# Optimization experiments

Measured on AMD Instinct MI355X. Metric: run time of the kernel, lower is better.

The kernel has to match this reference:

```python
import jax, jax.numpy as jnp
import numpy as np

B, T, H = 512, 200, 512


def setup_inputs() -> dict:
    key = jax.random.key(0)
    ks = jax.random.split(key, 9)
    s = 0.05  # small init to avoid gate saturation
    return {
        "inp": jax.random.normal(ks[0], (B, T), dtype=jnp.float32),
        "Wx1": jax.random.normal(ks[1], (1, 4 * H), dtype=jnp.float32) * s,
        "Wh1": jax.random.normal(ks[2], (H, 4 * H), dtype=jnp.float32) * s,
        "b1": jax.random.normal(ks[3], (4 * H,), dtype=jnp.float32) * s,
        "Wx2": jax.random.normal(ks[4], (H, 4 * H), dtype=jnp.float32) * s,
        "Wh2": jax.random.normal(ks[5], (H, 4 * H), dtype=jnp.float32) * s,
        "b2": jax.random.normal(ks[6], (4 * H,), dtype=jnp.float32) * s,
        "Wfc": jax.random.normal(ks[7], (H, 1), dtype=jnp.float32) * s,
        "bfc": jax.random.normal(ks[8], (1,), dtype=jnp.float32) * s,
    }


def _lstm(x_seq, Wx, Wh, b, h0, c0):
    # x_seq: [B, T, Din]; precompute input projection for all steps
    xz = jnp.einsum("btd,dg->btg", x_seq, Wx) + b  # [B, T, 4H]
    h_dim = Wh.shape[0]

    def step(carry, xz_t):
        h, c = carry
        z = xz_t + h @ Wh  # [B, 4H]
        i, f, g, o = jnp.split(z, 4, axis=-1)  # keras gate order i,f,g,o
        i = jax.nn.sigmoid(i)
        f = jax.nn.sigmoid(f)
        g = jnp.tanh(g)
        o = jax.nn.sigmoid(o)
        c = f * c + i * g
        h = o * jnp.tanh(c)
        return (h, c), h

    (hf, cf), hs = jax.lax.scan(step, (h0, c0), jnp.swapaxes(xz, 0, 1))
    return jnp.swapaxes(hs, 0, 1), hf, cf  # seq [B,T,H], final h, final c


def reference(inp, Wx1, Wh1, b1, Wx2, Wh2, b2, Wfc, bfc):
    b, t = inp.shape
    h = Wh1.shape[0]
    x = inp[..., None]  # [B, T, 1]
    z0 = jnp.zeros((b, h), dtype=inp.dtype)
    seq1, h1, c1 = _lstm(x, Wx1, Wh1, b1, z0, z0)
    # lstm2 is seeded with lstm1's final (h, c) because the [seq,h,c] list
    # is passed directly to the second keras LSTM layer
    seq2, h2, c2 = _lstm(seq1, Wx2, Wh2, b2, h1, c1)
    logits = h2 @ Wfc + bfc  # [B, 1]
    return logits
```

## Files before the change

kernel.cpp:

```cpp
#include <hip/hip_runtime.h>
#include <cstdio>

typedef __attribute__((ext_vector_type(8))) short short8;
typedef __attribute__((ext_vector_type(4))) float f32x4;
typedef unsigned long long u64;

#define MFMA16(a,b,c) __builtin_amdgcn_mfma_f32_16x16x32_bf16((a),(b),(c),0,0,0)
#define LOAD_SYS(p)    __hip_atomic_load((p), __ATOMIC_RELAXED, __HIP_MEMORY_SCOPE_SYSTEM)
#define STORE_SYS(p,v) __hip_atomic_store((p), (v), __ATOMIC_RELAXED, __HIP_MEMORY_SCOPE_SYSTEM)

typedef __attribute__((address_space(1))) unsigned AS1U;
typedef __attribute__((address_space(3))) unsigned AS3U;

constexpr size_t CNT_OFF = 0;
constexpr size_t HB_OFF  = 8192;
constexpr size_t PK1_OFF = HB_OFF + 1048576;
constexpr size_t PK2_OFF = PK1_OFF + 2097152;
constexpr size_t PKX_OFF = PK2_OFF + 2097152;
constexpr size_t SEQ_OFF = PKX_OFF + 2097152;
constexpr size_t WS_NEED = SEQ_OFF + 16ul * 200 * 32768;

__device__ __forceinline__ short f2bf(float f) {
  union { float f; unsigned u; } v; v.f = f;
  unsigned r = v.u + 0x7fffu + ((v.u >> 16) & 1u);
  return (short)(r >> 16);
}
__device__ __forceinline__ float bf2f(short s) {
  union { float f; unsigned u; } v; v.u = ((unsigned)(unsigned short)s) << 16;
  return v.f;
}
__device__ __forceinline__ float sigm(float x)   { return 1.f / (1.f + __expf(-x)); }
__device__ __forceinline__ float tanh_f(float x) { return 1.f - 2.f / (1.f + __expf(2.f * x)); }

__global__ void pack_w(const float* __restrict__ wh1, const float* __restrict__ wh2,
                       const float* __restrict__ wx2, unsigned char* __restrict__ ws)
{
  int tid = blockIdx.x * 256 + threadIdx.x;
  int m   = tid >> 16;
  int rem = tid & 65535;
  int k   = rem >> 7;
  int nf  = rem & 127;
  const float* W = (m == 0) ? wh1 : (m == 1) ? wh2 : wx2;
  short* dst = (short*)(ws + ((m == 0) ? PK1_OFF : (m == 1) ? PK2_OFF : PKX_OFF));
  int kf = k >> 5, sub = (k >> 3) & 3, e = k & 7;
  int base = ((nf * 16 + kf) * 64 + sub * 16) * 8 + e;
  const float* src = W + (size_t)k * 2048 + nf * 16;
#pragma unroll
  for (int c = 0; c < 16; ++c) dst[base + c * 8] = f2bf(src[c]);
}

__global__ __launch_bounds__(256, 1) void lstm_main(
    const float* __restrict__ inp, const float* __restrict__ Wx1,
    const float* __restrict__ b1,  const float* __restrict__ b2,
    const float* __restrict__ Wfc, const float* __restrict__ bfc,
    unsigned char* __restrict__ ws, float* __restrict__ out)
{
  __shared__ short8 ldsA[2048];
  __shared__ short8 ldsB[2048];
  __shared__ short8 bwx[4][2][8][64];
  __shared__ float  zlds[32][132];
  __shared__ unsigned short htile[32][36];
  __shared__ float  red[256];

  const int tid  = threadIdx.x;
  const int blk  = blockIdx.x;
  const int gr   = blk & 15;
  const int wj   = blk >> 4;
  const int w    = tid >> 6;
  const int lane = tid & 63;
  const int g0   = (w >> 1) << 1;
  const int cf   = w & 1;

  unsigned* fl = (unsigned*)(ws + CNT_OFF) + gr * 32;
  short8* hb0p = (short8*)(ws + HB_OFF) + (size_t)(0 * 16 + gr) * 2048;
  short8* hb1p = (short8*)(ws + HB_OFF) + (size_t)(1 * 16 + gr) * 2048;
  const short8* pk1 = (const short8*)(ws + PK1_OFF);
  const short8* pk2 = (const short8*)(ws + PK2_OFF);
  const short8* pkx = (const short8*)(ws + PKX_OFF);
  short8* seq = (short8*)(ws + SEQ_OFF) + (size_t)gr * (200 * 2048);

  short8 wh1f[2][16], wh2f[2][16], wxhi[2][8];
#pragma unroll
  for (int Gl = 0; Gl < 2; ++Gl) {
    int nf = (g0 + Gl) * 32 + wj * 2 + cf;
#pragma unroll
    for (int kf = 0; kf < 16; ++kf) {
      wh1f[Gl][kf] = pk1[(nf * 16 + kf) * 64 + lane];
      wh2f[Gl][kf] = pk2[(nf * 16 + kf) * 64 + lane];
    }
#pragma unroll
    for (int kf = 0; kf < 8; ++kf)
      bwx[w][Gl][kf][lane] = pkx[(nf * 16 + kf) * 64 + lane];
#pragma unroll
    for (int kf = 8; kf < 16; ++kf)
      wxhi[Gl][kf - 8] = pkx[(nf * 16 + kf) * 64 + lane];
  }

  const int hcol = tid & 31, rq = tid >> 5;
  const int jcol = wj * 32 + hcol;
  float wx1v[4], b1v[4], b2v[4];
#pragma unroll
  for (int G = 0; G < 4; ++G) {
    wx1v[G] = Wx1[G * 512 + jcol];
    b1v[G]  = b1[G * 512 + jcol];
    b2v[G]  = b2[G * 512 + jcol];
  }
  const float* xptr = inp + (size_t)(gr * 32 + rq * 4) * 200;

  const int pr = tid >> 3, pq = tid & 7;
  const int pc0 = wj * 32 + pq * 4;
  const int bq = ((((pc0 >> 5) * 2 + (pr >> 4)) * 64 + ((pc0 >> 3) & 3) * 16 + (pr & 15)) * 8
                  + (pc0 & 7)) >> 2;

  float cst1[4] = {0.f, 0.f, 0.f, 0.f};
  float cst2[4] = {0.f, 0.f, 0.f, 0.f};

  __syncthreads();

#pragma unroll 1
  for (int s = 0; s <= 200; ++s) {
    float xv[4];
    if (s < 200) {
#pragma unroll
      for (int i = 0; i < 4; ++i) xv[i] = xptr[i * 200 + s];
    }

    if (s > 0) {
      if (tid < 64) {
        const unsigned* fp = &fl[tid & 15];
        while (1) {
          unsigned v = LOAD_SYS((unsigned*)fp);
          if (__all((int)(v >= (unsigned)s))) break;
          __builtin_amdgcn_s_sleep(1);
        }
        asm volatile("" ::: "memory");
      }
    }
    __syncthreads();

    if (s >= 1) {
      const char* gsrc = (const char*)(seq + (size_t)(s - 1) * 2048);
      char* ldst = (char*)ldsA;
#pragma unroll
      for (int i = 0; i < 8; ++i)
        __builtin_amdgcn_global_load_lds(
            (const AS1U*)(gsrc + (w * 8 + i) * 1024 + lane * 16),
            (AS3U*)(ldst + (w * 8 + i) * 1024), 16, 0, 17 );
    }
    if (s >= 2) {
      const char* gsrc = (const char*)((s & 1) ? hb1p : hb0p);
      char* ldst = (char*)ldsB;
#pragma unroll
      for (int i = 0; i < 8; ++i)
        __builtin_amdgcn_global_load_lds(
            (const AS1U*)(gsrc + (w * 8 + i) * 1024 + lane * 16),
            (AS3U*)(ldst + (w * 8 + i) * 1024), 16, 0, 17);
    }
    __builtin_amdgcn_sched_barrier(0);
    if (s >= 2) asm volatile("s_waitcnt vmcnt(8)" ::: "memory");
    else        asm volatile("s_waitcnt vmcnt(0)" ::: "memory");
    __builtin_amdgcn_sched_barrier(0);
    __builtin_amdgcn_s_barrier();

    f32x4 acc1[2][2], acc2[2][2];
#pragma unroll
    for (int Gl = 0; Gl < 2; ++Gl)
#pragma unroll
      for (int m = 0; m < 2; ++m) {
        f32x4 z = {0.f, 0.f, 0.f, 0.f}; acc1[Gl][m] = z; acc2[Gl][m] = z;
      }

    if (s >= 1) {
#pragma unroll
      for (int m = 0; m < 2; ++m) {
#pragma unroll
        for (int kf = 0; kf < 16; ++kf) {
          short8 a = ldsA[(kf * 2 + m) * 64 + lane];
#pragma unroll
          for (int Gl = 0; Gl < 2; ++Gl) {
            if (s < 200) acc1[Gl][m] = MFMA16(a, wh1f[Gl][kf], acc1[Gl][m]);
            short8 bx = (kf < 8) ? bwx[w][Gl][kf][lane] : wxhi[Gl][kf - 8];
            acc2[Gl][m] = MFMA16(a, bx, acc2[Gl][m]);
          }
        }
      }
    }

    if (s < 200) {
#pragma unroll
      for (int Gl = 0; Gl < 2; ++Gl)
#pragma unroll
        for (int m = 0; m < 2; ++m)
#pragma unroll
          for (int r = 0; r < 4; ++r)
            zlds[m * 16 + (lane >> 4) * 4 + r][(g0 + Gl) * 32 + cf * 16 + (lane & 15)]
                = acc1[Gl][m][r];
    }
    __syncthreads();

    if (s < 200) {
#pragma unroll
      for (int i = 0; i < 4; ++i) {
        int row = rq * 4 + i;
        float zi = zlds[row][0 * 32 + hcol] + fmaf(xv[i], wx1v[0], b1v[0]);
        float zf = zlds[row][1 * 32 + hcol] + fmaf(xv[i], wx1v[1], b1v[1]);
        float zg = zlds[row][2 * 32 + hcol] + fmaf(xv[i], wx1v[2], b1v[2]);
        float zo = zlds[row][3 * 32 + hcol] + fmaf(xv[i], wx1v[3], b1v[3]);
        float cc = sigm(zf) * cst1[i] + sigm(zi) * tanh_f(zg);
        cst1[i] = cc;
        htile[row][hcol] = (unsigned short)f2bf(sigm(zo) * tanh_f(cc));
      }
    }

    if (s >= 2) {
#pragma unroll
      for (int m = 0; m < 2; ++m) {
#pragma unroll
        for (int kf = 0; kf < 16; ++kf) {
          short8 a = ldsB[(kf * 2 + m) * 64 + lane];
#pragma unroll
          for (int Gl = 0; Gl < 2; ++Gl)
            acc2[Gl][m] = MFMA16(a, wh2f[Gl][kf], acc2[Gl][m]);
        }
      }
    }
    __syncthreads();

    if (s < 200) {
      u64 hv = *(const u64*)&htile[pr][pq * 4];
      STORE_SYS((u64*)(seq + (size_t)s * 2048) + bq, hv);
    }

    if (s >= 1) {
#pragma unroll
      for (int Gl = 0; Gl < 2; ++Gl)
#pragma unroll
        for (int m = 0; m < 2; ++m)
#pragma unroll
          for (int r = 0; r < 4; ++r)
            zlds[m * 16 + (lane >> 4) * 4 + r][(g0 + Gl) * 32 + cf * 16 + (lane & 15)]
                = acc2[Gl][m][r];
    }
    __syncthreads();

    if (s >= 1) {
#pragma unroll
      for (int i = 0; i < 4; ++i) {
        int row = rq * 4 + i;
        float zi = zlds[row][0 * 32 + hcol] + b2v[0];
        float zf = zlds[row][1 * 32 + hcol] + b2v[1];
        float zg = zlds[row][2 * 32 + hcol] + b2v[2];
        float zo = zlds[row][3 * 32 + hcol] + b2v[3];
        float cc = sigm(zf) * cst2[i] + sigm(zi) * tanh_f(zg);
        cst2[i] = cc;
        htile[row][hcol] = (unsigned short)f2bf(sigm(zo) * tanh_f(cc));
      }
    }
    __syncthreads();

    if (s >= 1) {
      u64 hv = *(const u64*)&htile[pr][pq * 4];
      short8* dst = (s & 1) ? hb0p : hb1p;
      STORE_SYS((u64*)dst + bq, hv);
    }
    __syncthreads();
    if (tid == 0)
      STORE_SYS(&fl[wj], (unsigned)(s + 1));
  }

  if (wj == 0) {
    if (tid < 64) {
      const unsigned* fp = &fl[tid & 15];
      while (1) {
        unsigned v = LOAD_SYS((unsigned*)fp);
        if (__all((int)(v >= 201u))) break;
        __builtin_amdgcn_s_sleep(1);
      }
      asm volatile("" ::: "memory");
    }
    __syncthreads();

    const u64* h2 = (const u64*)hb1p;
    int r = tid >> 3, q = tid & 7;
    float sum = 0.f;
#pragma unroll
    for (int c = 0; c < 8; ++c) {
      int k0 = q * 64 + c * 8;
      int kf = k0 >> 5, sub = (k0 >> 3) & 3, m = r >> 4;
      int bq2 = ((kf * 2 + m) * 64 + sub * 16 + (r & 15)) * 2;
      union { u64 u[2]; unsigned short ss[8]; } cv;
      cv.u[0] = LOAD_SYS((u64*)h2 + bq2);
      cv.u[1] = LOAD_SYS((u64*)h2 + bq2 + 1);
#pragma unroll
      for (int e = 0; e < 8; ++e)
        sum = fmaf(bf2f((short)cv.ss[e]), Wfc[k0 + e], sum);
    }
    red[tid] = sum;
    __syncthreads();
    if (q == 0) {
      float o = bfc[0];
#pragma unroll
      for (int j = 0; j < 8; ++j) o += red[r * 8 + j];
      out[gr * 32 + r] = o;
    }
  }
}

extern "C" void kernel_launch(void* const* d_in, const int* in_sizes, int n_in,
                              void* d_out, int out_size, void* d_ws, size_t ws_size,
                              hipStream_t stream)
{
  if (ws_size < WS_NEED) {
    fprintf(stderr, "kernel_launch: ws_size %zu < needed %zu\n", ws_size, WS_NEED);
    return;
  }
  const float* inp = (const float*)d_in[0];
  const float* Wx1 = (const float*)d_in[1];
  const float* Wh1 = (const float*)d_in[2];
  const float* b1  = (const float*)d_in[3];
  const float* Wx2 = (const float*)d_in[4];
  const float* Wh2 = (const float*)d_in[5];
  const float* b2  = (const float*)d_in[6];
  const float* Wfc = (const float*)d_in[7];
  const float* bfc = (const float*)d_in[8];
  unsigned char* ws = (unsigned char*)d_ws;

  hipMemsetAsync(ws, 0, 8192, stream);
  pack_w<<<768, 256, 0, stream>>>(Wh1, Wh2, Wx2, ws);
  lstm_main<<<256, 256, 0, stream>>>(inp, Wx1, b1, b2, Wfc, bfc, ws, (float*)d_out);
}
```

Baseline: 1.451 ms.

## Split each block's batch tile into two ping-pong halves to overlap sync with compute

Each workgroup now handles two 16-row batch subgroups (A and B) instead of one 32-row group. It alternates phases, so one subgroup's global-to-LDS staging and cross-block wait overlap the other subgroup's MFMA and gate work. Layer-1 and layer-2 gate computations are also fused into a single pass per phase, cutting the number of barriers. Per-block flag arrays are replaced by one atomic counter per subgroup. The cost is half-height MFMA tiles, so the weight registers are reused less per step, and the per-step atomic counters may contend.

Measured after the change: 2.581 ms. 77.8% more time.

```diff
diff --git a/kernel.cpp b/kernel.cpp
--- a/kernel.cpp
+++ b/kernel.cpp
@@ -18,7 +18,7 @@
 constexpr size_t PK2_OFF = PK1_OFF + 2097152;
 constexpr size_t PKX_OFF = PK2_OFF + 2097152;
 constexpr size_t SEQ_OFF = PKX_OFF + 2097152;
-constexpr size_t WS_NEED = SEQ_OFF + 16ul * 200 * 32768;
+constexpr size_t WS_NEED = SEQ_OFF + 32ul * 200 * 16384;
 
 __device__ __forceinline__ short f2bf(float f) {
   union { float f; unsigned u; } v; v.f = f;
@@ -49,35 +49,144 @@
   for (int c = 0; c < 16; ++c) dst[base + c * 8] = f2bf(src[c]);
 }
 
+__device__ __forceinline__ void stage16k(const char* g, char* l, int w, int lane) {
+#pragma unroll
+  for (int i = 0; i < 4; ++i)
+    __builtin_amdgcn_global_load_lds(
+        (const AS1U*)(g + (w * 4 + i) * 1024 + lane * 16),
+        (AS3U*)(l + (w * 4 + i) * 1024), 16, 0, 17 );
+}
+
+#define LGKM_BAR() do { \
+  asm volatile("s_waitcnt lgkmcnt(0)" ::: "memory"); \
+  __builtin_amdgcn_s_barrier(); \
+  __builtin_amdgcn_sched_barrier(0); } while (0)
+
+__device__ __forceinline__ void phase_step(
+    int s, int tid, int lane, int w, int g0, int cf,
+    const short8* tA, const short8* tB,
+    const short8 (&wh1f)[2][16], const short8 (&wh2f)[2][16],
+    const short8 (&wxhi)[2][8], const short8 (&bwx)[4][2][8][64],
+    float (&zl1)[16][132], float (&zl2)[16][132],
+    unsigned short (&ht1)[16][36], unsigned short (&ht2)[16][36],
+    const float* xg, const float (&wx1v)[4], const float (&b1v)[4], const float (&b2v)[4],
+    float (&c1)[2], float (&c2)[2],
+    u64* seqG, u64* hbG0, u64* hbG1,
+    int pr, int pq, int bq, unsigned* cnt)
+{
+  f32x4 a1[2], a2[2];
+#pragma unroll
+  for (int Gl = 0; Gl < 2; ++Gl) { f32x4 z = {0.f,0.f,0.f,0.f}; a1[Gl] = z; a2[Gl] = z; }
+
+  if (s >= 1) {
+#pragma unroll
+    for (int kf = 0; kf < 16; ++kf) {
+      short8 a = tA[kf * 64 + lane];
+#pragma unroll
+      for (int Gl = 0; Gl < 2; ++Gl) {
+        if (s < 200) a1[Gl] = MFMA16(a, wh1f[Gl][kf], a1[Gl]);
+        short8 bxf = (kf < 8) ? bwx[w][Gl][kf][lane] : wxhi[Gl][kf - 8];
+        a2[Gl] = MFMA16(a, bxf, a2[Gl]);
+      }
+    }
+  }
+  if (s >= 2) {
+#pragma unroll
+    for (int kf = 0; kf < 16; ++kf) {
+      short8 b = tB[kf * 64 + lane];
+#pragma unroll
+      for (int Gl = 0; Gl < 2; ++Gl)
+        a2[Gl] = MFMA16(b, wh2f[Gl][kf], a2[Gl]);
+    }
+  }
+
+  {
+    int orow = (lane >> 4) * 4, oc = cf * 16 + (lane & 15);
+#pragma unroll
+    for (int Gl = 0; Gl < 2; ++Gl) {
+      int cc = (g0 + Gl) * 32 + oc;
+#pragma unroll
+      for (int r4 = 0; r4 < 4; ++r4) {
+        if (s >= 0 && s < 200)  zl1[orow + r4][cc] = a1[Gl][r4];
+        if (s >= 1 && s <= 200) zl2[orow + r4][cc] = a2[Gl][r4];
+      }
+    }
+  }
+  LGKM_BAR();
+
+  {
+    int hcol = tid & 31, rq = tid >> 5;
+#pragma unroll
+    for (int i = 0; i < 2; ++i) {
+      int row = rq * 2 + i;
+      if (s >= 0 && s < 200) {
+        float x  = xg[row * 200 + s];
+        float z0 = zl1[row][hcol]       + fmaf(x, wx1v[0], b1v[0]);
+        float z1 = zl1[row][32 + hcol]  + fmaf(x, wx1v[1], b1v[1]);
+        float z2 = zl1[row][64 + hcol]  + fmaf(x, wx1v[2], b1v[2]);
+        float z3 = zl1[row][96 + hcol]  + fmaf(x, wx1v[3], b1v[3]);
+        float cv = sigm(z1) * c1[i] + sigm(z0) * tanh_f(z2);
+        c1[i] = cv;
+        ht1[row][hcol] = (unsigned short)f2bf(sigm(z3) * tanh_f(cv));
+      }
+      if (s >= 1 && s <= 200) {
+        float z0 = zl2[row][hcol]       + b2v[0];
+        float z1 = zl2[row][32 + hcol]  + b2v[1];
+        float z2 = zl2[row][64 + hcol]  + b2v[2];
+        float z3 = zl2[row][96 + hcol]  + b2v[3];
+        float cv = sigm(z1) * c2[i] + sigm(z0) * tanh_f(z2);
+        c2[i] = cv;
+        ht2[row][hcol] = (unsigned short)f2bf(sigm(z3) * tanh_f(cv));
+      }
+    }
+  }
+  LGKM_BAR();
+
+  if (tid < 128) {
+    if (s >= 0 && s < 200)
+      STORE_SYS(seqG + (size_t)s * 2048 + bq, *(const u64*)&ht1[pr][pq * 4]);
+    if (s >= 1 && s <= 200)
+      STORE_SYS(((((s + 1) & 1) ? hbG1 : hbG0) + bq), *(const u64*)&ht2[pr][pq * 4]);
+  }
+  __syncthreads();
+  if (tid == 0 && s >= 0 && s <= 200)
+    __hip_atomic_fetch_add(cnt, 1u, __ATOMIC_RELAXED, __HIP_MEMORY_SCOPE_SYSTEM);
+}
+
 __global__ __launch_bounds__(256, 1) void lstm_main(
     const float* __restrict__ inp, const float* __restrict__ Wx1,
     const float* __restrict__ b1,  const float* __restrict__ b2,
     const float* __restrict__ Wfc, const float* __restrict__ bfc,
     unsigned char* __restrict__ ws, float* __restrict__ out)
 {
-  __shared__ short8 ldsA[2048];
-  __shared__ short8 ldsB[2048];
+  __shared__ short8 ldsAA[1024], ldsBA[1024];
+  __shared__ short8 ldsAB[1024], ldsBB[1024];
   __shared__ short8 bwx[4][2][8][64];
-  __shared__ float  zlds[32][132];
-  __shared__ unsigned short htile[32][36];
+  __shared__ float  zl1[16][132], zl2[16][132];
+  __shared__ unsigned short ht1[16][36], ht2[16][36];
   __shared__ float  red[256];
 
   const int tid  = threadIdx.x;
   const int blk  = blockIdx.x;
-  const int gr   = blk & 15;
-  const int wj   = blk >> 4;
+  const int p    = blk >> 4;
+  const int wj   = blk & 15;
+  const int grA  = 2 * p, grB = 2 * p + 1;
   const int w    = tid >> 6;
   const int lane = tid & 63;
   const int g0   = (w >> 1) << 1;
   const int cf   = w & 1;
 
-  unsigned* fl = (unsigned*)(ws + CNT_OFF) + gr * 32;
-  short8* hb0p = (short8*)(ws + HB_OFF) + (size_t)(0 * 16 + gr) * 2048;
-  short8* hb1p = (short8*)(ws + HB_OFF) + (size_t)(1 * 16 + gr) * 2048;
+  unsigned* cntA = (unsigned*)(ws + CNT_OFF) + grA * 32;
+  unsigned* cntB = (unsigned*)(ws + CNT_OFF) + grB * 32;
+  u64* hbA0 = (u64*)(ws + HB_OFF + (size_t)(0 * 32 + grA) * 16384);
+  u64* hbA1 = (u64*)(ws + HB_OFF + (size_t)(1 * 32 + grA) * 16384);
+  u64* hbB0 = (u64*)(ws + HB_OFF + (size_t)(0 * 32 + grB) * 16384);
+  u64* hbB1 = (u64*)(ws + HB_OFF + (size_t)(1 * 32 + grB) * 16384);
   const short8* pk1 = (const short8*)(ws + PK1_OFF);
   const short8* pk2 = (const short8*)(ws + PK2_OFF);
   const short8* pkx = (const short8*)(ws + PKX_OFF);
-  short8* seq = (short8*)(ws + SEQ_OFF) + (size_t)gr * (200 * 2048);
+  u64* seqA = (u64*)(ws + SEQ_OFF + (size_t)grA * 200 * 16384);
+  u64* seqB = (u64*)(ws + SEQ_OFF + (size_t)grB * 200 * 16384);
 
   short8 wh1f[2][16], wh2f[2][16], wxhi[2][8];
 #pragma unroll
@@ -96,7 +205,7 @@
       wxhi[Gl][kf - 8] = pkx[(nf * 16 + kf) * 64 + lane];
   }
 
-  const int hcol = tid & 31, rq = tid >> 5;
+  const int hcol = tid & 31;
   const int jcol = wj * 32 + hcol;
   float wx1v[4], b1v[4], b2v[4];
 #pragma unroll
@@ -105,189 +214,71 @@
     b1v[G]  = b1[G * 512 + jcol];
     b2v[G]  = b2[G * 512 + jcol];
   }
-  const float* xptr = inp + (size_t)(gr * 32 + rq * 4) * 200;
-
-  const int pr = tid >> 3, pq = tid & 7;
+  const float* xgA = inp + (size_t)(grA * 16) * 200;
+  const float* xgB = inp + (size_t)(grB * 16) * 200;
+
+  const int pr = (tid & 127) >> 3, pq = tid & 7;
   const int pc0 = wj * 32 + pq * 4;
-  const int bq = ((((pc0 >> 5) * 2 + (pr >> 4)) * 64 + ((pc0 >> 3) & 3) * 16 + (pr & 15)) * 8
-                  + (pc0 & 7)) >> 2;
-
-  float cst1[4] = {0.f, 0.f, 0.f, 0.f};
-  float cst2[4] = {0.f, 0.f, 0.f, 0.f};
+  const int bq = (((pc0 >> 5) * 64 + ((pc0 >> 3) & 3) * 16 + pr) * 8 + (pc0 & 7)) >> 2;
+
+  float cA1[2] = {0.f, 0.f}, cA2[2] = {0.f, 0.f};
+  float cB1[2] = {0.f, 0.f}, cB2[2] = {0.f, 0.f};
 
   __syncthreads();
 
 #pragma unroll 1
-  for (int s = 0; s <= 200; ++s) {
-    float xv[4];
-    if (s < 200) {
-#pragma unroll
-      for (int i = 0; i < 4; ++i) xv[i] = xptr[i * 200 + s];
-    }
-
-    if (s > 0) {
+  for (int r = 0; r <= 201; ++r) {
+    if (r >= 1 && r <= 200) {
       if (tid < 64) {
-        const unsigned* fp = &fl[tid & 15];
-        while (1) {
-          unsigned v = LOAD_SYS((unsigned*)fp);
-          if (__all((int)(v >= (unsigned)s))) break;
-          __builtin_amdgcn_s_sleep(1);
-        }
+        while ((int)LOAD_SYS(cntA) < 16 * r) __builtin_amdgcn_s_sleep(1);
         asm volatile("" ::: "memory");
       }
     }
     __syncthreads();
 
-    if (s >= 1) {
-      const char* gsrc = (const char*)(seq + (size_t)(s - 1) * 2048);
-      char* ldst = (char*)ldsA;
-#pragma unroll
-      for (int i = 0; i < 8; ++i)
-        __builtin_amdgcn_global_load_lds(
-            (const AS1U*)(gsrc + (w * 8 + i) * 1024 + lane * 16),
-            (AS3U*)(ldst + (w * 8 + i) * 1024), 16, 0, 17 );
-    }
-    if (s >= 2) {
-      const char* gsrc = (const char*)((s & 1) ? hb1p : hb0p);
-      char* ldst = (char*)ldsB;
-#pragma unroll
-      for (int i = 0; i < 8; ++i)
-        __builtin_amdgcn_global_load_lds(
-            (const AS1U*)(gsrc + (w * 8 + i) * 1024 + lane * 16),
-            (AS3U*)(ldst + (w * 8 + i) * 1024), 16, 0, 17);
-    }
-    __builtin_amdgcn_sched_barrier(0);
-    if (s >= 2) asm volatile("s_waitcnt vmcnt(8)" ::: "memory");
-    else        asm volatile("s_waitcnt vmcnt(0)" ::: "memory");
-    __builtin_amdgcn_sched_barrier(0);
-    __builtin_amdgcn_s_barrier();
-
-    f32x4 acc1[2][2], acc2[2][2];
-#pragma unroll
-    for (int Gl = 0; Gl < 2; ++Gl)
-#pragma unroll
-      for (int m = 0; m < 2; ++m) {
-        f32x4 z = {0.f, 0.f, 0.f, 0.f}; acc1[Gl][m] = z; acc2[Gl][m] = z;
-      }
-
-    if (s >= 1) {
-#pragma unroll
-      for (int m = 0; m < 2; ++m) {
-#pragma unroll
-        for (int kf = 0; kf < 16; ++kf) {
-          short8 a = ldsA[(kf * 2 + m) * 64 + lane];
-#pragma unroll
-          for (int Gl = 0; Gl < 2; ++Gl) {
-            if (s < 200) acc1[Gl][m] = MFMA16(a, wh1f[Gl][kf], acc1[Gl][m]);
-            short8 bx = (kf < 8) ? bwx[w][Gl][kf][lane] : wxhi[Gl][kf - 8];
-            acc2[Gl][m] = MFMA16(a, bx, acc2[Gl][m]);
-          }
-        }
-      }
-    }
-
-    if (s < 200) {
-#pragma unroll
-      for (int Gl = 0; Gl < 2; ++Gl)
-#pragma unroll
-        for (int m = 0; m < 2; ++m)
-#pragma unroll
-          for (int r = 0; r < 4; ++r)
-            zlds[m * 16 + (lane >> 4) * 4 + r][(g0 + Gl) * 32 + cf * 16 + (lane & 15)]
-                = acc1[Gl][m][r];
+    if (r >= 1 && r <= 200)
+      stage16k((const char*)seqA + (size_t)(r - 1) * 16384, (char*)ldsAA, w, lane);
+    if (r >= 2 && r <= 200)
+      stage16k((const char*)((r & 1) ? hbA1 : hbA0), (char*)ldsBA, w, lane);
+
+    phase_step(r - 1, tid, lane, w, g0, cf, ldsAB, ldsBB,
+               wh1f, wh2f, wxhi, bwx, zl1, zl2, ht1, ht2,
+               xgB, wx1v, b1v, b2v, cB1, cB2, seqB, hbB0, hbB1, pr, pq, bq, cntB);
+
+    if (r >= 1 && r <= 200) {
+      if (tid < 64) {
+        while ((int)LOAD_SYS(cntB) < 16 * r) __builtin_amdgcn_s_sleep(1);
+        asm volatile("" ::: "memory");
+      }
     }
     __syncthreads();
 
-    if (s < 200) {
-#pragma unroll
-      for (int i = 0; i < 4; ++i) {
-        int row = rq * 4 + i;
-        float zi = zlds[row][0 * 32 + hcol] + fmaf(xv[i], wx1v[0], b1v[0]);
-        float zf = zlds[row][1 * 32 + hcol] + fmaf(xv[i], wx1v[1], b1v[1]);
-        float zg = zlds[row][2 * 32 + hcol] + fmaf(xv[i], wx1v[2], b1v[2]);
-        float zo = zlds[row][3 * 32 + hcol] + fmaf(xv[i], wx1v[3], b1v[3]);
-        float cc = sigm(zf) * cst1[i] + sigm(zi) * tanh_f(zg);
-        cst1[i] = cc;
-        htile[row][hcol] = (unsigned short)f2bf(sigm(zo) * tanh_f(cc));
-      }
-    }
-
-    if (s >= 2) {
-#pragma unroll
-      for (int m = 0; m < 2; ++m) {
-#pragma unroll
-        for (int kf = 0; kf < 16; ++kf) {
-          short8 a = ldsB[(kf * 2 + m) * 64 + lane];
-#pragma unroll
-          for (int Gl = 0; Gl < 2; ++Gl)
-            acc2[Gl][m] = MFMA16(a, wh2f[Gl][kf], acc2[Gl][m]);
-        }
-      }
-    }
-    __syncthreads();
-
-    if (s < 200) {
-      u64 hv = *(const u64*)&htile[pr][pq * 4];
-      STORE_SYS((u64*)(seq + (size_t)s * 2048) + bq, hv);
-    }
-
-    if (s >= 1) {
-#pragma unroll
-      for (int Gl = 0; Gl < 2; ++Gl)
-#pragma unroll
-        for (int m = 0; m < 2; ++m)
-#pragma unroll
-          for (int r = 0; r < 4; ++r)
-            zlds[m * 16 + (lane >> 4) * 4 + r][(g0 + Gl) * 32 + cf * 16 + (lane & 15)]
-                = acc2[Gl][m][r];
-    }
-    __syncthreads();
-
-    if (s >= 1) {
-#pragma unroll
-      for (int i = 0; i < 4; ++i) {
-        int row = rq * 4 + i;
-        float zi = zlds[row][0 * 32 + hcol] + b2v[0];
-        float zf = zlds[row][1 * 32 + hcol] + b2v[1];
-        float zg = zlds[row][2 * 32 + hcol] + b2v[2];
-        float zo = zlds[row][3 * 32 + hcol] + b2v[3];
-        float cc = sigm(zf) * cst2[i] + sigm(zi) * tanh_f(zg);
-        cst2[i] = cc;
-        htile[row][hcol] = (unsigned short)f2bf(sigm(zo) * tanh_f(cc));
-      }
-    }
-    __syncthreads();
-
-    if (s >= 1) {
-      u64 hv = *(const u64*)&htile[pr][pq * 4];
-      short8* dst = (s & 1) ? hb0p : hb1p;
-      STORE_SYS((u64*)dst + bq, hv);
-    }
-    __syncthreads();
-    if (tid == 0)
-      STORE_SYS(&fl[wj], (unsigned)(s + 1));
+    if (r >= 1 && r <= 200)
+      stage16k((const char*)seqB + (size_t)(r - 1) * 16384, (char*)ldsAB, w, lane);
+    if (r >= 2 && r <= 200)
+      stage16k((const char*)((r & 1) ? hbB1 : hbB0), (char*)ldsBB, w, lane);
+
+    phase_step(r, tid, lane, w, g0, cf, ldsAA, ldsBA,
+               wh1f, wh2f, wxhi, bwx, zl1, zl2, ht1, ht2,
+               xgA, wx1v, b1v, b2v, cA1, cA2, seqA, hbA0, hbA1, pr, pq, bq, cntA);
   }
 
   if (wj == 0) {
     if (tid < 64) {
-      const unsigned* fp = &fl[tid & 15];
-      while (1) {
-        unsigned v = LOAD_SYS((unsigned*)fp);
-        if (__all((int)(v >= 201u))) break;
-        __builtin_amdgcn_s_sleep(1);
-      }
+      while ((int)LOAD_SYS(cntA) < 16 * 201) __builtin_amdgcn_s_sleep(1);
+      while ((int)LOAD_SYS(cntB) < 16 * 201) __builtin_amdgcn_s_sleep(1);
       asm volatile("" ::: "memory");
     }
     __syncthreads();
 
-    const u64* h2 = (const u64*)hb1p;
-    int r = tid >> 3, q = tid & 7;
+    int r2 = tid >> 3, q = tid & 7;
+    int row = r2 & 15;
+    const u64* h2 = (r2 < 16) ? hbA1 : hbB1;
     float sum = 0.f;
 #pragma unroll
     for (int c = 0; c < 8; ++c) {
       int k0 = q * 64 + c * 8;
-      int kf = k0 >> 5, sub = (k0 >> 3) & 3, m = r >> 4;
-      int bq2 = ((kf * 2 + m) * 64 + sub * 16 + (r & 15)) * 2;
+      int bq2 = ((k0 >> 5) * 64 + ((k0 >> 3) & 3) * 16 + row) * 2;
       union { u64 u[2]; unsigned short ss[8]; } cv;
       cv.u[0] = LOAD_SYS((u64*)h2 + bq2);
       cv.u[1] = LOAD_SYS((u64*)h2 + bq2 + 1);
@@ -300,8 +291,9 @@
     if (q == 0) {
       float o = bfc[0];
 #pragma unroll
-      for (int j = 0; j < 8; ++j) o += red[r * 8 + j];
-      out[gr * 32 + r] = o;
+      for (int j = 0; j < 8; ++j) o += red[r2 * 8 + j];
+      int gr = (r2 < 16) ? grA : grB;
+      out[gr * 16 + row] = o;
     }
   }
 }
```

## Merge layer epilogues into one phase and cut per-step barriers

Applied to the files above, without the earlier changes.

Reorders each timestep so both layers' matmuls finish before a single combined gate epilogue. Layer-2 pre-activations are stored to LDS as bf16, and both h tiles are written out together by 128 threads. Each wave now publishes its own progress flag after its stores drain, replacing one flag set after an extra block barrier. The seq loads switch to the default cache policy. The goal is fewer block-wide barriers and serialized phases on the recurrent critical path, at the cost of rounding layer-2 gate sums to bf16, which may reduce accuracy.

Measured after the change: 1.735 ms. 1.2x slower.

```diff
diff --git a/kernel.cpp b/kernel.cpp
--- a/kernel.cpp
+++ b/kernel.cpp
@@ -49,6 +49,26 @@
   for (int c = 0; c < 16; ++c) dst[base + c * 8] = f2bf(src[c]);
 }
 
+__device__ __forceinline__ void stage32k_cached(const char* g, char* l, int w, int lane) {
+#pragma unroll
+  for (int i = 0; i < 8; ++i)
+    __builtin_amdgcn_global_load_lds(
+        (const AS1U*)(g + (w * 8 + i) * 1024 + lane * 16),
+        (AS3U*)(l + (w * 8 + i) * 1024), 16, 0, 0 );
+}
+__device__ __forceinline__ void stage32k_llc(const char* g, char* l, int w, int lane) {
+#pragma unroll
+  for (int i = 0; i < 8; ++i)
+    __builtin_amdgcn_global_load_lds(
+        (const AS1U*)(g + (w * 8 + i) * 1024 + lane * 16),
+        (AS3U*)(l + (w * 8 + i) * 1024), 16, 0, 17 );
+}
+
+#define LGKM_BAR() do { \
+  asm volatile("s_waitcnt lgkmcnt(0)" ::: "memory"); \
+  __builtin_amdgcn_s_barrier(); \
+  __builtin_amdgcn_sched_barrier(0); } while (0)
+
 __global__ __launch_bounds__(256, 1) void lstm_main(
     const float* __restrict__ inp, const float* __restrict__ Wx1,
     const float* __restrict__ b1,  const float* __restrict__ b2,
@@ -58,8 +78,10 @@
   __shared__ short8 ldsA[2048];
   __shared__ short8 ldsB[2048];
   __shared__ short8 bwx[4][2][8][64];
-  __shared__ float  zlds[32][132];
-  __shared__ unsigned short htile[32][36];
+  __shared__ float  zl1[32][132];
+  __shared__ unsigned short zl2[32][132];
+  __shared__ unsigned short ht1[32][36];
+  __shared__ unsigned short ht2[32][36];
   __shared__ float  red[256];
 
   const int tid  = threadIdx.x;
@@ -72,12 +94,12 @@
   const int cf   = w & 1;
 
   unsigned* fl = (unsigned*)(ws + CNT_OFF) + gr * 32;
-  short8* hb0p = (short8*)(ws + HB_OFF) + (size_t)(0 * 16 + gr) * 2048;
-  short8* hb1p = (short8*)(ws + HB_OFF) + (size_t)(1 * 16 + gr) * 2048;
+  u64* hbU0 = (u64*)(ws + HB_OFF + (size_t)(0 * 16 + gr) * 32768);
+  u64* hbU1 = (u64*)(ws + HB_OFF + (size_t)(1 * 16 + gr) * 32768);
   const short8* pk1 = (const short8*)(ws + PK1_OFF);
   const short8* pk2 = (const short8*)(ws + PK2_OFF);
   const short8* pkx = (const short8*)(ws + PKX_OFF);
-  short8* seq = (short8*)(ws + SEQ_OFF) + (size_t)gr * (200 * 2048);
+  u64* seqU = (u64*)(ws + SEQ_OFF + (size_t)gr * 200 * 32768);
 
   short8 wh1f[2][16], wh2f[2][16], wxhi[2][8];
 #pragma unroll
@@ -107,10 +129,13 @@
   }
   const float* xptr = inp + (size_t)(gr * 32 + rq * 4) * 200;
 
-  const int pr = tid >> 3, pq = tid & 7;
-  const int pc0 = wj * 32 + pq * 4;
-  const int bq = ((((pc0 >> 5) * 2 + (pr >> 4)) * 64 + ((pc0 >> 3) & 3) * 16 + (pr & 15)) * 8
-                  + (pc0 & 7)) >> 2;
+  const int spr = tid >> 2, spqa = (tid & 3) * 2, spqb = spqa + 1;
+  auto bqof = [&](int pq) {
+    int pc0 = wj * 32 + pq * 4;
+    return ((((pc0 >> 5) * 2 + (spr >> 4)) * 64 + ((pc0 >> 3) & 3) * 16 + (spr & 15)) * 8
+            + (pc0 & 7)) >> 2;
+  };
+  const int bqa = bqof(spqa), bqb = bqof(spqb);
 
   float cst1[4] = {0.f, 0.f, 0.f, 0.f};
   float cst2[4] = {0.f, 0.f, 0.f, 0.f};
@@ -126,8 +151,8 @@
     }
 
     if (s > 0) {
-      if (tid < 64) {
-        const unsigned* fp = &fl[tid & 15];
+      if (tid < 32) {
+        const unsigned* fp = &fl[tid];
         while (1) {
           unsigned v = LOAD_SYS((unsigned*)fp);
           if (__all((int)(v >= (unsigned)s))) break;
@@ -138,29 +163,16 @@
     }
     __syncthreads();
 
-    if (s >= 1) {
-      const char* gsrc = (const char*)(seq + (size_t)(s - 1) * 2048);
-      char* ldst = (char*)ldsA;
-#pragma unroll
-      for (int i = 0; i < 8; ++i)
-        __builtin_amdgcn_global_load_lds(
-            (const AS1U*)(gsrc + (w * 8 + i) * 1024 + lane * 16),
-            (AS3U*)(ldst + (w * 8 + i) * 1024), 16, 0, 17 );
-    }
-    if (s >= 2) {
-      const char* gsrc = (const char*)((s & 1) ? hb1p : hb0p);
-      char* ldst = (char*)ldsB;
-#pragma unroll
-      for (int i = 0; i < 8; ++i)
-        __builtin_amdgcn_global_load_lds(
-            (const AS1U*)(gsrc + (w * 8 + i) * 1024 + lane * 16),
-            (AS3U*)(ldst + (w * 8 + i) * 1024), 16, 0, 17);
-    }
+    if (s >= 1)
+      stage32k_cached((const char*)(seqU + (size_t)(s - 1) * 4096), (char*)ldsA, w, lane);
+    if (s >= 2)
+      stage32k_llc((const char*)((s & 1) ? hbU1 : hbU0), (char*)ldsB, w, lane);
     __builtin_amdgcn_sched_barrier(0);
     if (s >= 2) asm volatile("s_waitcnt vmcnt(8)" ::: "memory");
     else        asm volatile("s_waitcnt vmcnt(0)" ::: "memory");
     __builtin_amdgcn_sched_barrier(0);
     __builtin_amdgcn_s_barrier();
+    __builtin_amdgcn_sched_barrier(0);
 
     f32x4 acc1[2][2], acc2[2][2];
 #pragma unroll
@@ -186,91 +198,85 @@
       }
     }
 
-    if (s < 200) {
-#pragma unroll
-      for (int Gl = 0; Gl < 2; ++Gl)
+    asm volatile("s_waitcnt vmcnt(0)" ::: "memory");
+    __builtin_amdgcn_sched_barrier(0);
+    __builtin_amdgcn_s_barrier();
+    __builtin_amdgcn_sched_barrier(0);
+
+    if (s >= 2) {
+#pragma unroll
+      for (int m = 0; m < 2; ++m) {
+#pragma unroll
+        for (int kf = 0; kf < 16; ++kf) {
+          short8 b = ldsB[(kf * 2 + m) * 64 + lane];
+#pragma unroll
+          for (int Gl = 0; Gl < 2; ++Gl)
+            acc2[Gl][m] = MFMA16(b, wh2f[Gl][kf], acc2[Gl][m]);
+        }
+      }
+    }
+
+    {
+      int orow = (lane >> 4) * 4, oc = cf * 16 + (lane & 15);
+#pragma unroll
+      for (int Gl = 0; Gl < 2; ++Gl) {
+        int cc = (g0 + Gl) * 32 + oc;
 #pragma unroll
         for (int m = 0; m < 2; ++m)
 #pragma unroll
-          for (int r = 0; r < 4; ++r)
-            zlds[m * 16 + (lane >> 4) * 4 + r][(g0 + Gl) * 32 + cf * 16 + (lane & 15)]
-                = acc1[Gl][m][r];
-    }
-    __syncthreads();
-
-    if (s < 200) {
-#pragma unroll
-      for (int i = 0; i < 4; ++i) {
-        int row = rq * 4 + i;
-        float zi = zlds[row][0 * 32 + hcol] + fmaf(xv[i], wx1v[0], b1v[0]);
-        float zf = zlds[row][1 * 32 + hcol] + fmaf(xv[i], wx1v[1], b1v[1]);
-        float zg = zlds[row][2 * 32 + hcol] + fmaf(xv[i], wx1v[2], b1v[2]);
-        float zo = zlds[row][3 * 32 + hcol] + fmaf(xv[i], wx1v[3], b1v[3]);
-        float cc = sigm(zf) * cst1[i] + sigm(zi) * tanh_f(zg);
+          for (int r4 = 0; r4 < 4; ++r4) {
+            int row = m * 16 + orow + r4;
+            if (s < 200)  zl1[row][cc] = acc1[Gl][m][r4];
+            if (s >= 1)   zl2[row][cc] = (unsigned short)f2bf(acc2[Gl][m][r4]);
+          }
+      }
+    }
+    LGKM_BAR();
+
+#pragma unroll
+    for (int i = 0; i < 4; ++i) {
+      int row = rq * 4 + i;
+      if (s < 200) {
+        float z0 = zl1[row][hcol]      + fmaf(xv[i], wx1v[0], b1v[0]);
+        float z1 = zl1[row][32 + hcol] + fmaf(xv[i], wx1v[1], b1v[1]);
+        float z2 = zl1[row][64 + hcol] + fmaf(xv[i], wx1v[2], b1v[2]);
+        float z3 = zl1[row][96 + hcol] + fmaf(xv[i], wx1v[3], b1v[3]);
+        float cc = sigm(z1) * cst1[i] + sigm(z0) * tanh_f(z2);
         cst1[i] = cc;
-        htile[row][hcol] = (unsigned short)f2bf(sigm(zo) * tanh_f(cc));
-      }
-    }
-
-    if (s >= 2) {
-#pragma unroll
-      for (int m = 0; m < 2; ++m) {
-#pragma unroll
-        for (int kf = 0; kf < 16; ++kf) {
-          short8 a = ldsB[(kf * 2 + m) * 64 + lane];
-#pragma unroll
-          for (int Gl = 0; Gl < 2; ++Gl)
-            acc2[Gl][m] = MFMA16(a, wh2f[Gl][kf], acc2[Gl][m]);
-        }
-      }
-    }
-    __syncthreads();
-
-    if (s < 200) {
-      u64 hv = *(const u64*)&htile[pr][pq * 4];
-      STORE_SYS((u64*)(seq + (size_t)s * 2048) + bq, hv);
-    }
-
-    if (s >= 1) {
-#pragma unroll
-      for (int Gl = 0; Gl < 2; ++Gl)
-#pragma unroll
-        for (int m = 0; m < 2; ++m)
-#pragma unroll
-          for (int r = 0; r < 4; ++r)
-            zlds[m * 16 + (lane >> 4) * 4 + r][(g0 + Gl) * 32 + cf * 16 + (lane & 15)]
-                = acc2[Gl][m][r];
-    }
-    __syncthreads();
-
-    if (s >= 1) {
-#pragma unroll
-      for (int i = 0; i < 4; ++i) {
-        int row = rq * 4 + i;
-        float zi = zlds[row][0 * 32 + hcol] + b2v[0];
-        float zf = zlds[row][1 * 32 + hcol] + b2v[1];
-        float zg = zlds[row][2 * 32 + hcol] + b2v[2];
-        float zo = zlds[row][3 * 32 + hcol] + b2v[3];
-        float cc = sigm(zf) * cst2[i] + sigm(zi) * tanh_f(zg);
+        ht1[row][hcol] = (unsigned short)f2bf(sigm(z3) * tanh_f(cc));
+      }
+      if (s >= 1) {
+        float z0 = bf2f((short)zl2[row][hcol])      + b2v[0];
+        float z1 = bf2f((short)zl2[row][32 + hcol]) + b2v[1];
+        float z2 = bf2f((short)zl2[row][64 + hcol]) + b2v[2];
+        float z3 = bf2f((short)zl2[row][96 + hcol]) + b2v[3];
+        float cc = sigm(z1) * cst2[i] + sigm(z0) * tanh_f(z2);
         cst2[i] = cc;
-        htile[row][hcol] = (unsigned short)f2bf(sigm(zo) * tanh_f(cc));
-      }
-    }
-    __syncthreads();
-
-    if (s >= 1) {
-      u64 hv = *(const u64*)&htile[pr][pq * 4];
-      short8* dst = (s & 1) ? hb0p : hb1p;
-      STORE_SYS((u64*)dst + bq, hv);
-    }
-    __syncthreads();
-    if (tid == 0)
-      STORE_SYS(&fl[wj], (unsigned)(s + 1));
+        ht2[row][hcol] = (unsigned short)f2bf(sigm(z3) * tanh_f(cc));
+      }
+    }
+    LGKM_BAR();
+
+    if (tid < 128) {
+      if (s < 200) {
+        u64* d = seqU + (size_t)s * 4096;
+        STORE_SYS(d + bqa, *(const u64*)&ht1[spr][spqa * 4]);
+        STORE_SYS(d + bqb, *(const u64*)&ht1[spr][spqb * 4]);
+      }
+      if (s >= 1) {
+        u64* d = ((s + 1) & 1) ? hbU1 : hbU0;
+        STORE_SYS(d + bqa, *(const u64*)&ht2[spr][spqa * 4]);
+        STORE_SYS(d + bqb, *(const u64*)&ht2[spr][spqb * 4]);
+      }
+      asm volatile("s_waitcnt vmcnt(0)" ::: "memory");
+      if ((tid & 63) == 0)
+        STORE_SYS(&fl[(tid >> 6) * 16 + wj], (unsigned)(s + 1));
+    }
   }
 
   if (wj == 0) {
-    if (tid < 64) {
-      const unsigned* fp = &fl[tid & 15];
+    if (tid < 32) {
+      const unsigned* fp = &fl[tid];
       while (1) {
         unsigned v = LOAD_SYS((unsigned*)fp);
         if (__all((int)(v >= 201u))) break;
@@ -280,17 +286,16 @@
     }
     __syncthreads();
 
-    const u64* h2 = (const u64*)hb1p;
-    int r = tid >> 3, q = tid & 7;
+    int r2 = tid >> 3, q = tid & 7;
     float sum = 0.f;
 #pragma unroll
     for (int c = 0; c < 8; ++c) {
       int k0 = q * 64 + c * 8;
-      int kf = k0 >> 5, sub = (k0 >> 3) & 3, m = r >> 4;
-      int bq2 = ((kf * 2 + m) * 64 + sub * 16 + (r & 15)) * 2;
+      int kf = k0 >> 5, sub = (k0 >> 3) & 3, m = r2 >> 4;
+      int bq2 = ((kf * 2 + m) * 64 + sub * 16 + (r2 & 15)) * 2;
       union { u64 u[2]; unsigned short ss[8]; } cv;
-      cv.u[0] = LOAD_SYS((u64*)h2 + bq2);
-      cv.u[1] = LOAD_SYS((u64*)h2 + bq2 + 1);
+      cv.u[0] = LOAD_SYS(hbU1 + bq2);
+      cv.u[1] = LOAD_SYS(hbU1 + bq2 + 1);
 #pragma unroll
       for (int e = 0; e < 8; ++e)
         sum = fmaf(bf2f((short)cv.ss[e]), Wfc[k0 + e], sum);
@@ -300,8 +305,8 @@
     if (q == 0) {
       float o = bfc[0];
 #pragma unroll
-      for (int j = 0; j < 8; ++j) o += red[r * 8 + j];
-      out[gr * 32 + r] = o;
+      for (int j = 0; j < 8; ++j) o += red[r2 * 8 + j];
+      out[gr * 32 + r2] = o;
     }
   }
 }
```
